# Kernel optimization log

Measured on AMD Instinct MI355X. Metric: run time of the kernel, lower is better.

The kernel has to match this reference:

```python
import jax, jax.numpy as jnp
import numpy as np
import math

H = 512       # hidden_dim
NL = 4        # num_layers
N2 = 32       # d_state // 2
B, L = 8, 4096
DT_MIN, DT_MAX = 1e-3, 1e-1
EPS = 1e-5


def _layer_norm(x, gamma, beta):
    mu = jnp.mean(x, axis=-1, keepdims=True)
    var = jnp.mean(jnp.square(x - mu), axis=-1, keepdims=True)
    return (x - mu) * jax.lax.rsqrt(var + EPS) * gamma + beta


def setup_inputs() -> dict:
    key = jax.random.key(0)
    ks = jax.random.split(key, 8)
    x = jax.random.normal(ks[0], (B, L, H), dtype=jnp.float32)
    # S4DKernel buffers / params, stacked over layers
    log_dt = jax.random.uniform(ks[1], (NL, H)) * (math.log(DT_MAX) - math.log(DT_MIN)) + math.log(DT_MIN)
    A_imag = jnp.broadcast_to(math.pi * jnp.arange(N2, dtype=jnp.float32), (NL, H, N2)).copy()
    log_A_real = jnp.full((NL, H, N2), math.log(0.5), dtype=jnp.float32)
    C = jax.random.normal(ks[2], (NL, H, N2, 2), dtype=jnp.float32)  # view_as_real of cfloat
    D = jax.random.normal(ks[3], (NL, H), dtype=jnp.float32)
    # 1x1 Conv1d h -> 2h (pointwise linear over channels)
    W = jax.random.normal(ks[4], (NL, 2 * H, H), dtype=jnp.float32) / math.sqrt(H)
    b = jax.random.normal(ks[5], (NL, 2 * H), dtype=jnp.float32) * 0.01
    gamma = jnp.ones((NL, H), dtype=jnp.float32)
    beta = jnp.zeros((NL, H), dtype=jnp.float32)
    return dict(x=x, log_dt=log_dt, A_imag=A_imag, log_A_real=log_A_real,
                C=C, D=D, W=W, b=b, gamma=gamma, beta=beta)


def reference(x, log_dt, A_imag, log_A_real, C, D, W, b, gamma, beta):
    Bsz, Lseq, h = x.shape
    t = jnp.arange(Lseq, dtype=jnp.float32)
    for i in range(NL):
        # --- S4D kernel generation ---
        dt = jnp.exp(log_dt[i])                                    # (h,)
        Cc = C[i, ..., 0] + 1j * C[i, ..., 1]                      # (h, n)
        A = -jnp.exp(log_A_real[i]) + 1j * A_imag[i]               # (h, n)
        dA = A * dt[:, None]                                       # (h, n)
        Cmod = Cc * (jnp.exp(dA) - 1.0) / A                        # (h, n)
        # Vandermonde: exp(dA * l), reduced over state dim
        K = 2.0 * jnp.einsum('hn,hnl->hl', Cmod,
                             jnp.exp(dA[:, :, None] * t)).real     # (h, L)
        # --- FFT long convolution ---
        u = jnp.transpose(x, (0, 2, 1))                            # (B, h, L)
        kf = jnp.fft.rfft(K, n=2 * Lseq)                           # (h, L+1)
        uf = jnp.fft.rfft(u, n=2 * Lseq)                           # (B, h, L+1)
        y = jnp.fft.irfft(uf * kf, n=2 * Lseq)[..., :Lseq]         # (B, h, L)
        y = y + u * D[i][:, None]
        y = jax.nn.gelu(y, approximate=False)                      # torch nn.GELU default (erf)
        # 1x1 conv h -> 2h then GLU over channel dim
        z = jnp.einsum('oh,bhl->bol', W[i], y) + b[i][None, :, None]
        a, g = jnp.split(z, 2, axis=1)
        y = a * jax.nn.sigmoid(g)                                  # (B, h, L)
        y = jnp.transpose(y, (0, 2, 1))                            # (B, L, h)
        x = _layer_norm(y + x, gamma[i], beta[i])
    return x
```

## Files before the change

kernel.cpp:

```cpp
#include <hip/hip_runtime.h>
#include <hip/hip_bf16.h>
#include <math.h>

#define H 512
#define NL 4
#define N2 32
#define Bsz 8
#define Lseq 4096
#define BT (Bsz*Lseq)
#define LC2 64
#define NCC (BT/LC2)
#define CPB (Lseq/LC2)

typedef __attribute__((ext_vector_type(8))) short short8;
typedef __attribute__((ext_vector_type(4))) float float4v;


__device__ __forceinline__ float bf2f(unsigned short u) {
    union { unsigned int i; float f; } x; x.i = ((unsigned int)u) << 16; return x.f;
}
__device__ __forceinline__ unsigned short f2bf(float f) {
    union { float f; unsigned int i; } x; x.f = f;
    unsigned int u = x.i + 0x7fff + ((x.i >> 16) & 1);
    return (unsigned short)(u >> 16);
}
__device__ __forceinline__ uint2 pack4bf(float a, float b, float c, float d) {
    uint2 r;
    r.x = (unsigned)f2bf(a) | ((unsigned)f2bf(b) << 16);
    r.y = (unsigned)f2bf(c) | ((unsigned)f2bf(d) << 16);
    return r;
}
__device__ __forceinline__ void async_copy16(const void* g, void* l) {
    __builtin_amdgcn_global_load_lds(
        (const __attribute__((address_space(1))) void*)g,
        (__attribute__((address_space(3))) void*)l, 16, 0, 0);
}

__global__ void wconv_kernel(const float* __restrict__ W, unsigned short* __restrict__ Wbf) {
    int tid = blockIdx.x * 256 + threadIdx.x;
    Wbf[tid] = f2bf(W[tid]);
}

__global__ void params_kernel(const float* __restrict__ log_dt, const float* __restrict__ A_imag,
                              const float* __restrict__ log_A_real, const float* __restrict__ Cin,
                              float* __restrict__ dA, float* __restrict__ Ct) {
    int tid = blockIdx.x * 256 + threadIdx.x;
    int h = tid % H;
    int n = (tid / H) % N2;
    int layer = tid / (H * N2);
    float dt = expf(log_dt[layer * H + h]);
    int pidx = (layer * H + h) * N2 + n;
    float Are = -expf(log_A_real[pidx]);
    float Aim = A_imag[pidx];
    float dre = Are * dt, dim = Aim * dt;
    float er = expf(dre);
    float lre = er * cosf(dim), lim = er * sinf(dim);
    float nre = lre - 1.0f, nim = lim;
    float inv = 1.0f / (Are * Are + Aim * Aim);
    float tre = (nre * Are + nim * Aim) * inv;
    float tim = (nim * Are - nre * Aim) * inv;
    float Ccre = Cin[pidx * 2], Ccim = Cin[pidx * 2 + 1];
    int oidx = ((layer * N2 + n) * 2) * H + h;
    dA[oidx] = dre;  dA[oidx + H] = dim;
    Ct[oidx] = 2.0f * (Ccre * tre - Ccim * tim);
    Ct[oidx + H] = 2.0f * (Ccre * tim + Ccim * tre);
}

__global__ void kergen_k_kernel(const float* __restrict__ dA, const float* __restrict__ Ct,
                                unsigned short* __restrict__ kmat) {
    int t = blockIdx.x * 256 + threadIdx.x;
    int d = t & 63;
    int h = (t >> 6) & (H - 1);
    int layer = t >> 15;
    float fd = (float)d;
    float sum = 0.f;
    for (int n = 0; n < N2; n++) {
        int base = ((layer * N2 + n) * 2) * H + h;
        float dre = dA[base], dim = dA[base + H];
        float Ctr = Ct[base], Cti = Ct[base + H];
        float e = expf(dre * fd);
        sum += Ctr * e * cosf(dim * fd) - Cti * e * sinf(dim * fd);
    }
    kmat[t] = f2bf(sum);
}

__global__ void kergenW_kernel(const float* __restrict__ dA, unsigned short* __restrict__ Wst, int layer) {
    int t = blockIdx.x * 256 + threadIdx.x;
    int j = t & 63;
    int r = (t >> 6) & 63;
    int h = t >> 12;
    int n = r >> 1;
    int base = ((layer * N2 + n) * 2) * H + h;
    float dre = dA[base], dim = dA[base + H];
    float p = (float)(63 - j);
    float e = expf(dre * p);
    Wst[t] = f2bf((r & 1) ? e * sinf(dim * p) : e * cosf(dim * p));
}

__global__ void kergenV_kernel(const float* __restrict__ dA, const float* __restrict__ Ct,
                               unsigned short* __restrict__ Vl, int layer) {
    int t = blockIdx.x * 256 + threadIdx.x;
    int c2 = t & 63;
    int l = (t >> 6) & 63;
    int h = t >> 12;
    int n = c2 >> 1;
    int base = ((layer * N2 + n) * 2) * H + h;
    float dre = dA[base], dim = dA[base + H];
    float Ctr = Ct[base], Cti = Ct[base + H];
    float q = (float)(l + 1);
    float e = expf(dre * q);
    float ar = e * cosf(dim * q), ai = e * sinf(dim * q);
    float vre = Ctr * ar - Cti * ai;
    float vim = Ctr * ai + Cti * ar;
    Vl[t] = f2bf((c2 & 1) ? -vim : vre);
}

__global__ __launch_bounds__(256) void t1_f32_kernel(const float* __restrict__ xi,
                                                     unsigned short* __restrict__ ut) {
    __shared__ float tile[64][68];
    int bx = blockIdx.x;
    int pt = bx & 511, ht = bx >> 9;
    int p0 = pt * 64, h0 = ht * 64;
    int t = threadIdx.x;
    int jr = t & 15, ib = t >> 4;
#pragma unroll
    for (int pass = 0; pass < 4; pass++) {
        int i = ib + pass * 16;
        float4 v = *(const float4*)(xi + (size_t)(p0 + i) * H + h0 + jr * 4);
        *(float4*)(&tile[i][jr * 4]) = v;
    }
    __syncthreads();
#pragma unroll
    for (int pass = 0; pass < 4; pass++) {
        int i2 = ib + pass * 16;
        int j2 = jr * 4;
        uint2 pk = pack4bf(tile[j2][i2], tile[j2 + 1][i2], tile[j2 + 2][i2], tile[j2 + 3][i2]);
        *(uint2*)(ut + (size_t)(h0 + i2) * BT + p0 + j2) = pk;
    }
}

__global__ __launch_bounds__(256) void states_kernel(const unsigned short* __restrict__ ut,
                                                     const unsigned short* __restrict__ Wst,
                                                     unsigned short* __restrict__ Sloc) {
    int h = blockIdx.x;
    int wave = threadIdx.x >> 6, lane = threadIdx.x & 63;
    int r16 = lane & 15, quad = lane >> 4;
    const unsigned short* uh = ut + (size_t)h * BT;
    const unsigned short* wh = Wst + (size_t)h * 64 * 64;
    unsigned short* sh = Sloc + (size_t)h * NCC * 64;
    for (int nt = 0; nt < 8; nt++) {
        int cc0 = wave * 128 + nt * 16;
        float4v acc[4] = {};
#pragma unroll
        for (int k0 = 0; k0 < 64; k0 += 32) {
            short8 bf = *reinterpret_cast<const short8*>(uh + (size_t)(cc0 + r16) * 64 + k0 + quad * 8);
#pragma unroll
            for (int mt = 0; mt < 4; mt++) {
                short8 af = *reinterpret_cast<const short8*>(wh + (mt * 16 + r16) * 64 + k0 + quad * 8);
                acc[mt] = __builtin_amdgcn_mfma_f32_16x16x32_bf16(af, bf, acc[mt], 0, 0, 0);
            }
        }
        int cc = cc0 + r16;
#pragma unroll
        for (int mt = 0; mt < 4; mt++) {
            uint2 pk = pack4bf(acc[mt][0], acc[mt][1], acc[mt][2], acc[mt][3]);
            *(uint2*)(sh + (size_t)cc * 64 + mt * 16 + quad * 4) = pk;
        }
    }
}

__global__ void combine_kernel(unsigned short* __restrict__ Sloc, const float* __restrict__ dA, int layer) {
    int t = blockIdx.x * 256 + threadIdx.x;
    int n = t & 31;
    int b = (t >> 5) & 7;
    int h = t >> 8;
    int base = ((layer * N2 + n) * 2) * H + h;
    float dre = dA[base], dim = dA[base + H];
    float e = expf(dre * 64.f);
    float Lr = e * cosf(dim * 64.f), Li = e * sinf(dim * 64.f);
    unsigned int* p = (unsigned int*)Sloc + ((size_t)h * NCC + b * CPB) * 32 + n;
    float sr = 0.f, si = 0.f;
    for (int c = 0; c < CPB; c++) {
        unsigned int v = p[(size_t)c * 32];
        float pr = bf2f(v & 0xffff), pi = bf2f(v >> 16);
        p[(size_t)c * 32] = (unsigned)f2bf(sr) | ((unsigned)f2bf(si) << 16);
        float nr = fmaf(Lr, sr, fmaf(-Li, si, pr));
        float ni = fmaf(Lr, si, fmaf(Li, sr, pi));
        sr = nr; si = ni;
    }
}

__global__ __launch_bounds__(256) void conv_kernel(const unsigned short* __restrict__ ut,
                                                   const unsigned short* __restrict__ kmat,
                                                   const unsigned short* __restrict__ Vl,
                                                   const unsigned short* __restrict__ Sent,
                                                   const float* __restrict__ Dp,
                                                   unsigned short* __restrict__ yt, int layer) {
    __shared__ unsigned short T[64][72];
    int h = blockIdx.x, half = blockIdx.y;
    int t = threadIdx.x;
    const unsigned short* km = kmat + ((size_t)layer * H + h) * 64;
    {
        int l = t >> 2, j0 = (t & 3) * 16;
#pragma unroll
        for (int g = 0; g < 2; g++) {
            short8 v;
#pragma unroll
            for (int e = 0; e < 8; e++) {
                int j = j0 + g * 8 + e;
                v[e] = (j <= l) ? (short)km[l - j] : (short)0;
            }
            *reinterpret_cast<short8*>(&T[l][j0 + g * 8]) = v;
        }
    }
    __syncthreads();
    int wave = t >> 6, lane = t & 63;
    int r16 = lane & 15, quad = lane >> 4;
    const unsigned short* uh = ut + (size_t)h * BT;
    const unsigned short* vh = Vl + (size_t)h * 64 * 64;
    const unsigned short* eh = Sent + (size_t)h * NCC * 64;
    unsigned short* yh = yt + (size_t)h * BT;
    float Dh = Dp[layer * H + h];
    for (int nt = 0; nt < 4; nt++) {
        int cc0 = half * 256 + wave * 64 + nt * 16;
        float4v acc[4] = {};
#pragma unroll
        for (int k0 = 0; k0 < 64; k0 += 32) {
            short8 bf = *reinterpret_cast<const short8*>(uh + (size_t)(cc0 + r16) * 64 + k0 + quad * 8);
#pragma unroll
            for (int mt = 0; mt < 4; mt++) {
                short8 af = *reinterpret_cast<const short8*>(&T[mt * 16 + r16][k0 + quad * 8]);
                acc[mt] = __builtin_amdgcn_mfma_f32_16x16x32_bf16(af, bf, acc[mt], 0, 0, 0);
            }
        }
#pragma unroll
        for (int k0 = 0; k0 < 64; k0 += 32) {
            short8 bf = *reinterpret_cast<const short8*>(eh + (size_t)(cc0 + r16) * 64 + k0 + quad * 8);
#pragma unroll
            for (int mt = 0; mt < 4; mt++) {
                short8 af = *reinterpret_cast<const short8*>(vh + (mt * 16 + r16) * 64 + k0 + quad * 8);
                acc[mt] = __builtin_amdgcn_mfma_f32_16x16x32_bf16(af, bf, acc[mt], 0, 0, 0);
            }
        }
        int cc = cc0 + r16;
#pragma unroll
        for (int mt = 0; mt < 4; mt++) {
            size_t p = (size_t)cc * 64 + mt * 16 + quad * 4;
            ushort4 uu = *(const ushort4*)(uh + p);
            float o[4];
#pragma unroll
            for (int r = 0; r < 4; r++) {
                float y = acc[mt][r] + Dh * bf2f(((const unsigned short*)&uu)[r]);
                o[r] = 0.5f * y * (1.0f + erff(y * 0.70710678118654752f));
            }
            *(uint2*)(yh + p) = pack4bf(o[0], o[1], o[2], o[3]);
        }
    }
}

__global__ __launch_bounds__(256) void transpose2_kernel(const unsigned short* __restrict__ yt,
                                                         unsigned short* __restrict__ yb) {
    __shared__ unsigned short tile[64][72];
    int bx = blockIdx.x;
    int pt = bx & 511, ht = bx >> 9;
    int p0 = pt * 64, h0 = ht * 64;
    int t = threadIdx.x;
    int jr = t & 7, ib = t >> 3;
#pragma unroll
    for (int pass = 0; pass < 2; pass++) {
        int i = ib + pass * 32;
        short8 v = *reinterpret_cast<const short8*>(yt + (size_t)(h0 + i) * BT + p0 + jr * 8);
        *reinterpret_cast<short8*>(&tile[i][jr * 8]) = v;
    }
    __syncthreads();
    int pp = t >> 2, hg = t & 3;
    short8 o0, o1;
#pragma unroll
    for (int r = 0; r < 8; r++) o0[r] = (short)tile[hg * 16 + r][pp];
#pragma unroll
    for (int r = 0; r < 8; r++) o1[r] = (short)tile[hg * 16 + 8 + r][pp];
    unsigned short* dst = yb + (size_t)(p0 + pp) * H + h0 + hg * 16;
    *reinterpret_cast<short8*>(dst) = o0;
    *reinterpret_cast<short8*>(dst + 8) = o1;
}

__global__ __launch_bounds__(256) void gemm_glu_kernel(const unsigned short* __restrict__ ybf,
                                                       const unsigned short* __restrict__ Wbf,
                                                       const float* __restrict__ bias,
                                                       unsigned short* __restrict__ yo, int layer) {
    __shared__ unsigned short As[3][128 * 32];
    __shared__ unsigned short Bs[3][128 * 32];
    int tid = threadIdx.x;
    int wave = tid >> 6, lane = tid & 63;
    int wr = wave >> 1, wc = wave & 1;
    int r16 = lane & 15, quad = lane >> 4;
    int m0 = blockIdx.x * 128;
    int o0 = blockIdx.y * 64;
    const unsigned short* Wl = Wbf + (size_t)layer * 2 * H * H;

    int srow = lane >> 2;
    int scol = ((lane & 3) ^ ((srow >> 1) & 3)) * 8;
    const unsigned short* aS0 = ybf + ((size_t)(m0 + wave * 16 + srow)) * H + scol;
    const unsigned short* aS1 = aS0 + (size_t)64 * H;
    const unsigned short* bSA = Wl + ((size_t)(o0 + wave * 16 + srow)) * H + scol;
    const unsigned short* bSG = bSA + (size_t)512 * H;
    const int aoff0 = (wave * 16) * 32;
    const int aoff1 = (64 + wave * 16) * 32;

    int rcol = (quad ^ ((r16 >> 1) & 3)) * 8;

    float4v acc_a[4][2] = {}, acc_g[4][2] = {};

    async_copy16(aS0,      &As[0][aoff0]);
    async_copy16(aS1,      &As[0][aoff1]);
    async_copy16(bSA,      &Bs[0][aoff0]);
    async_copy16(bSG,      &Bs[0][aoff1]);
    async_copy16(aS0 + 32, &As[1][aoff0]);
    async_copy16(aS1 + 32, &As[1][aoff1]);
    async_copy16(bSA + 32, &Bs[1][aoff0]);
    async_copy16(bSG + 32, &Bs[1][aoff1]);
    asm volatile("s_waitcnt vmcnt(4)" ::: "memory");
    __builtin_amdgcn_s_barrier();

#pragma unroll
    for (int ks = 0; ks < 16; ++ks) {
        const int b = ks % 3;
        if (ks < 14) {
            const int nb = (ks + 2) % 3;
            const int kn = (ks + 2) * 32;
            async_copy16(aS0 + kn, &As[nb][aoff0]);
            async_copy16(aS1 + kn, &As[nb][aoff1]);
            async_copy16(bSA + kn, &Bs[nb][aoff0]);
            async_copy16(bSG + kn, &Bs[nb][aoff1]);
        }

        short8 af[4], ba[2], bg[2];
#pragma unroll
        for (int mi = 0; mi < 4; mi++)
            af[mi] = *reinterpret_cast<const short8*>(&As[b][(wr * 64 + mi * 16 + r16) * 32 + rcol]);
#pragma unroll
        for (int ni = 0; ni < 2; ni++) {
            ba[ni] = *reinterpret_cast<const short8*>(&Bs[b][(wc * 32 + ni * 16 + r16) * 32 + rcol]);
            bg[ni] = *reinterpret_cast<const short8*>(&Bs[b][(64 + wc * 32 + ni * 16 + r16) * 32 + rcol]);
        }
#pragma unroll
        for (int mi = 0; mi < 4; mi++)
#pragma unroll
            for (int ni = 0; ni < 2; ni++) {
                acc_a[mi][ni] = __builtin_amdgcn_mfma_f32_16x16x32_bf16(af[mi], ba[ni], acc_a[mi][ni], 0, 0, 0);
                acc_g[mi][ni] = __builtin_amdgcn_mfma_f32_16x16x32_bf16(af[mi], bg[ni], acc_g[mi][ni], 0, 0, 0);
            }

        if (ks < 14) {
            asm volatile("s_waitcnt vmcnt(4) lgkmcnt(0)" ::: "memory");
            __builtin_amdgcn_s_barrier();
        } else if (ks == 14) {
            asm volatile("s_waitcnt vmcnt(0) lgkmcnt(0)" ::: "memory");
            __builtin_amdgcn_s_barrier();
        }
    }

    const float* bl = bias + layer * 2 * H;
#pragma unroll
    for (int ni = 0; ni < 2; ni++) {
        int o = o0 + wc * 32 + ni * 16 + r16;
        float ba_ = bl[o], bg_ = bl[H + o];
#pragma unroll
        for (int mi = 0; mi < 4; mi++)
#pragma unroll
            for (int r = 0; r < 4; r++) {
                int l = m0 + wr * 64 + mi * 16 + quad * 4 + r;
                float av = acc_a[mi][ni][r] + ba_;
                float gv = acc_g[mi][ni][r] + bg_;
                yo[(size_t)l * H + o] = f2bf(av * (1.0f / (1.0f + expf(-gv))));
            }
    }
}

__global__ __launch_bounds__(256) void ln_t_kernel(const unsigned short* __restrict__ yo,
                                                   const float* __restrict__ xf,
                                                   const unsigned short* __restrict__ xb,
                                                   const float* __restrict__ gamma,
                                                   const float* __restrict__ beta,
                                                   unsigned short* __restrict__ xR,
                                                   unsigned short* __restrict__ ut,
                                                   int in_f32, int layer) {
    __shared__ unsigned short tl[64][520];
    int t = threadIdx.x;
    int p0 = blockIdx.x * 64;
    int lane8 = t & 7;
    int rowb = t >> 3;
    const float* gl = gamma + layer * H;
    const float* bl = beta + layer * H;
#pragma unroll
    for (int rr = 0; rr < 2; rr++) {
        int row = rowb + rr * 32;
        size_t gbase = (size_t)(p0 + row) * H;
        float v[64];
        float s = 0.f, s2 = 0.f;
#pragma unroll
        for (int cc = 0; cc < 8; cc++) {
            int h0 = (lane8 + cc * 8) * 8;
            short8 yv = *reinterpret_cast<const short8*>(yo + gbase + h0);
            if (in_f32) {
                float4 x0 = *(const float4*)(xf + gbase + h0);
                float4 x1 = *(const float4*)(xf + gbase + h0 + 4);
                v[cc * 8 + 0] = bf2f((unsigned short)yv[0]) + x0.x;
                v[cc * 8 + 1] = bf2f((unsigned short)yv[1]) + x0.y;
                v[cc * 8 + 2] = bf2f((unsigned short)yv[2]) + x0.z;
                v[cc * 8 + 3] = bf2f((unsigned short)yv[3]) + x0.w;
                v[cc * 8 + 4] = bf2f((unsigned short)yv[4]) + x1.x;
                v[cc * 8 + 5] = bf2f((unsigned short)yv[5]) + x1.y;
                v[cc * 8 + 6] = bf2f((unsigned short)yv[6]) + x1.z;
                v[cc * 8 + 7] = bf2f((unsigned short)yv[7]) + x1.w;
            } else {
                short8 xv = *reinterpret_cast<const short8*>(xb + gbase + h0);
#pragma unroll
                for (int i = 0; i < 8; i++)
                    v[cc * 8 + i] = bf2f((unsigned short)yv[i]) + bf2f((unsigned short)xv[i]);
            }
#pragma unroll
            for (int i = 0; i < 8; i++) { s += v[cc * 8 + i]; s2 = fmaf(v[cc * 8 + i], v[cc * 8 + i], s2); }
        }
        s += __shfl_xor(s, 1);  s2 += __shfl_xor(s2, 1);
        s += __shfl_xor(s, 2);  s2 += __shfl_xor(s2, 2);
        s += __shfl_xor(s, 4);  s2 += __shfl_xor(s2, 4);
        float mu = s * (1.0f / H);
        float var = s2 * (1.0f / H) - mu * mu;
        float inv = rsqrtf(var + 1e-5f);
#pragma unroll
        for (int cc = 0; cc < 8; cc++) {
            int h0 = (lane8 + cc * 8) * 8;
            float4 g0 = *(const float4*)(gl + h0);
            float4 g1 = *(const float4*)(gl + h0 + 4);
            float4 b0 = *(const float4*)(bl + h0);
            float4 b1 = *(const float4*)(bl + h0 + 4);
            short8 pk;
            pk[0] = (short)f2bf((v[cc * 8 + 0] - mu) * inv * g0.x + b0.x);
            pk[1] = (short)f2bf((v[cc * 8 + 1] - mu) * inv * g0.y + b0.y);
            pk[2] = (short)f2bf((v[cc * 8 + 2] - mu) * inv * g0.z + b0.z);
            pk[3] = (short)f2bf((v[cc * 8 + 3] - mu) * inv * g0.w + b0.w);
            pk[4] = (short)f2bf((v[cc * 8 + 4] - mu) * inv * g1.x + b1.x);
            pk[5] = (short)f2bf((v[cc * 8 + 5] - mu) * inv * g1.y + b1.y);
            pk[6] = (short)f2bf((v[cc * 8 + 6] - mu) * inv * g1.z + b1.z);
            pk[7] = (short)f2bf((v[cc * 8 + 7] - mu) * inv * g1.w + b1.w);
            *reinterpret_cast<short8*>(xR + gbase + h0) = pk;
            *reinterpret_cast<short8*>(&tl[row][h0]) = pk;
        }
    }
    __syncthreads();
#pragma unroll
    for (int hh = 0; hh < 2; hh++) {
        int h = t + hh * 256;
        unsigned short* dst = ut + (size_t)h * BT + p0;
#pragma unroll
        for (int pc = 0; pc < 8; pc++) {
            short8 o;
#pragma unroll
            for (int e = 0; e < 8; e++) o[e] = (short)tl[pc * 8 + e][h];
            *reinterpret_cast<short8*>(dst + pc * 8) = o;
        }
    }
}

__global__ __launch_bounds__(256) void ln_kernel(const unsigned short* __restrict__ yo,
                                                 const float* __restrict__ xf,
                                                 const unsigned short* __restrict__ xb,
                                                 const float* __restrict__ gamma, const float* __restrict__ beta,
                                                 float* __restrict__ of, unsigned short* __restrict__ ob,
                                                 int in_f32, int out_f32, int layer) {
    int wave = threadIdx.x >> 6, lane = threadIdx.x & 63;
    size_t row = (size_t)blockIdx.x * 4 + wave;
    const unsigned short* yp = yo + row * H + lane * 8;
    short8 yv = *reinterpret_cast<const short8*>(yp);
    float v[8];
    if (in_f32) {
        const float* xp = xf + row * H + lane * 8;
        float4 x0 = *(const float4*)(xp);
        float4 x1 = *(const float4*)(xp + 4);
        v[0] = bf2f((unsigned short)yv[0]) + x0.x; v[1] = bf2f((unsigned short)yv[1]) + x0.y;
        v[2] = bf2f((unsigned short)yv[2]) + x0.z; v[3] = bf2f((unsigned short)yv[3]) + x0.w;
        v[4] = bf2f((unsigned short)yv[4]) + x1.x; v[5] = bf2f((unsigned short)yv[5]) + x1.y;
        v[6] = bf2f((unsigned short)yv[6]) + x1.z; v[7] = bf2f((unsigned short)yv[7]) + x1.w;
    } else {
        const unsigned short* xp = xb + row * H + lane * 8;
        short8 xv = *reinterpret_cast<const short8*>(xp);
#pragma unroll
        for (int i = 0; i < 8; i++)
            v[i] = bf2f((unsigned short)yv[i]) + bf2f((unsigned short)xv[i]);
    }
    float s = 0.f, s2 = 0.f;
#pragma unroll
    for (int i = 0; i < 8; i++) { s += v[i]; s2 = fmaf(v[i], v[i], s2); }
#pragma unroll
    for (int off = 32; off; off >>= 1) {
        s += __shfl_xor(s, off);
        s2 += __shfl_xor(s2, off);
    }
    float mu = s * (1.0f / H);
    float var = s2 * (1.0f / H) - mu * mu;
    float inv = rsqrtf(var + 1e-5f);
    const float* gl = gamma + layer * H + lane * 8;
    const float* bl = beta + layer * H + lane * 8;
    float o[8];
#pragma unroll
    for (int i = 0; i < 8; i++)
        o[i] = (v[i] - mu) * inv * gl[i] + bl[i];
    if (out_f32) {
        float* op = of + row * H + lane * 8;
        *(float4*)(op) = make_float4(o[0], o[1], o[2], o[3]);
        *(float4*)(op + 4) = make_float4(o[4], o[5], o[6], o[7]);
    } else {
        unsigned short* op = ob + row * H + lane * 8;
        uint2 p0 = pack4bf(o[0], o[1], o[2], o[3]);
        uint2 p1 = pack4bf(o[4], o[5], o[6], o[7]);
        *(uint2*)(op) = p0;
        *(uint2*)(op + 4) = p1;
    }
}

extern "C" void kernel_launch(void* const* d_in, const int* in_sizes, int n_in,
                              void* d_out, int out_size, void* d_ws, size_t ws_size,
                              hipStream_t stream) {
    const float* x          = (const float*)d_in[0];
    const float* log_dt     = (const float*)d_in[1];
    const float* A_imag     = (const float*)d_in[2];
    const float* log_A_real = (const float*)d_in[3];
    const float* C          = (const float*)d_in[4];
    const float* D          = (const float*)d_in[5];
    const float* W          = (const float*)d_in[6];
    const float* bias       = (const float*)d_in[7];
    const float* gamma      = (const float*)d_in[8];
    const float* beta       = (const float*)d_in[9];

    char* ws = (char*)d_ws;
    unsigned short* xR   = (unsigned short*)(ws + 0);
    unsigned short* Sloc = (unsigned short*)(ws + 67108864);
    unsigned short* u_t  = (unsigned short*)(ws + 100663296);
    unsigned short* ybf  = (unsigned short*)(ws + 100663296);
    unsigned short* y_t  = (unsigned short*)(ws + 134217728);
    unsigned short* yo   = (unsigned short*)(ws + 134217728);
    unsigned short* Wbf  = (unsigned short*)(ws + 167772160);
    unsigned short* WV   = (unsigned short*)(ws + 171966464);
    unsigned short* kmat = (unsigned short*)(ws + 176160768);
    float*          dA   = (float*)(ws + 176422912);
    float*          Ct   = (float*)(ws + 176947200);
    float* xout_final    = (float*)d_out;

    wconv_kernel<<<NL * 2 * H * H / 256, 256, 0, stream>>>(W, Wbf);
    params_kernel<<<NL * N2 * H / 256, 256, 0, stream>>>(log_dt, A_imag, log_A_real, C, dA, Ct);
    kergen_k_kernel<<<NL * H * 64 / 256, 256, 0, stream>>>(dA, Ct, kmat);

    for (int layer = 0; layer < NL; ++layer) {
        if (layer == 0)
            t1_f32_kernel<<<4096, 256, 0, stream>>>(x, u_t);
        kergenW_kernel<<<H * 64 * 64 / 256, 256, 0, stream>>>(dA, WV, layer);
        states_kernel<<<H, 256, 0, stream>>>(u_t, WV, Sloc);
        combine_kernel<<<H * Bsz * N2 / 256, 256, 0, stream>>>(Sloc, dA, layer);
        kergenV_kernel<<<H * 64 * 64 / 256, 256, 0, stream>>>(dA, Ct, WV, layer);
        conv_kernel<<<dim3(H, 2), 256, 0, stream>>>(u_t, kmat, WV, Sloc, D, y_t, layer);
        transpose2_kernel<<<4096, 256, 0, stream>>>(y_t, ybf);
        gemm_glu_kernel<<<dim3(BT / 128, H / 64), 256, 0, stream>>>(ybf, Wbf, bias, yo, layer);
        if (layer < NL - 1) {
            ln_t_kernel<<<BT / 64, 256, 0, stream>>>(yo, x, xR, gamma, beta,
                                                     xR, u_t, (layer == 0) ? 1 : 0, layer);
        } else {
            ln_kernel<<<BT / 4, 256, 0, stream>>>(yo, x, xR, gamma, beta,
                                                  xout_final, xR, 0, 1, layer);
        }
    }
}
```

Baseline: 854.3 us.

## Fuse chunk-state, scan combine and convolution into one per-(channel,batch) SSM kernel

Replaces the separate states, combine and conv kernels with a single ssm_kernel launched per channel and batch. Chunk-local states are computed with MFMA into shared memory, one wave runs the serial complex scan across the 64 chunks (real/imag pairs split over lanes and exchanged with shuffles), and the result feeds the intra/inter-chunk MFMA convolution directly. This removes the global Sloc round trips and two launches. In exchange, the scan runs serially on a single wave while the other waves wait at a barrier, and W and V now need separate buffers.

Result: no change. 841.3 us (-1.5%).

```diff
diff --git a/kernel.cpp b/kernel.cpp
--- a/kernel.cpp
+++ b/kernel.cpp
@@ -139,65 +139,17 @@
     }
 }
 
-__global__ __launch_bounds__(256) void states_kernel(const unsigned short* __restrict__ ut,
-                                                     const unsigned short* __restrict__ Wst,
-                                                     unsigned short* __restrict__ Sloc) {
-    int h = blockIdx.x;
-    int wave = threadIdx.x >> 6, lane = threadIdx.x & 63;
-    int r16 = lane & 15, quad = lane >> 4;
-    const unsigned short* uh = ut + (size_t)h * BT;
-    const unsigned short* wh = Wst + (size_t)h * 64 * 64;
-    unsigned short* sh = Sloc + (size_t)h * NCC * 64;
-    for (int nt = 0; nt < 8; nt++) {
-        int cc0 = wave * 128 + nt * 16;
-        float4v acc[4] = {};
-#pragma unroll
-        for (int k0 = 0; k0 < 64; k0 += 32) {
-            short8 bf = *reinterpret_cast<const short8*>(uh + (size_t)(cc0 + r16) * 64 + k0 + quad * 8);
-#pragma unroll
-            for (int mt = 0; mt < 4; mt++) {
-                short8 af = *reinterpret_cast<const short8*>(wh + (mt * 16 + r16) * 64 + k0 + quad * 8);
-                acc[mt] = __builtin_amdgcn_mfma_f32_16x16x32_bf16(af, bf, acc[mt], 0, 0, 0);
-            }
-        }
-        int cc = cc0 + r16;
-#pragma unroll
-        for (int mt = 0; mt < 4; mt++) {
-            uint2 pk = pack4bf(acc[mt][0], acc[mt][1], acc[mt][2], acc[mt][3]);
-            *(uint2*)(sh + (size_t)cc * 64 + mt * 16 + quad * 4) = pk;
-        }
-    }
-}
-
-__global__ void combine_kernel(unsigned short* __restrict__ Sloc, const float* __restrict__ dA, int layer) {
-    int t = blockIdx.x * 256 + threadIdx.x;
-    int n = t & 31;
-    int b = (t >> 5) & 7;
-    int h = t >> 8;
-    int base = ((layer * N2 + n) * 2) * H + h;
-    float dre = dA[base], dim = dA[base + H];
-    float e = expf(dre * 64.f);
-    float Lr = e * cosf(dim * 64.f), Li = e * sinf(dim * 64.f);
-    unsigned int* p = (unsigned int*)Sloc + ((size_t)h * NCC + b * CPB) * 32 + n;
-    float sr = 0.f, si = 0.f;
-    for (int c = 0; c < CPB; c++) {
-        unsigned int v = p[(size_t)c * 32];
-        float pr = bf2f(v & 0xffff), pi = bf2f(v >> 16);
-        p[(size_t)c * 32] = (unsigned)f2bf(sr) | ((unsigned)f2bf(si) << 16);
-        float nr = fmaf(Lr, sr, fmaf(-Li, si, pr));
-        float ni = fmaf(Lr, si, fmaf(Li, sr, pi));
-        sr = nr; si = ni;
-    }
-}
-
-__global__ __launch_bounds__(256) void conv_kernel(const unsigned short* __restrict__ ut,
-                                                   const unsigned short* __restrict__ kmat,
-                                                   const unsigned short* __restrict__ Vl,
-                                                   const unsigned short* __restrict__ Sent,
-                                                   const float* __restrict__ Dp,
-                                                   unsigned short* __restrict__ yt, int layer) {
+__global__ __launch_bounds__(256) void ssm_kernel(const unsigned short* __restrict__ ut,
+                                                  const unsigned short* __restrict__ kmat,
+                                                  const unsigned short* __restrict__ Wst,
+                                                  const unsigned short* __restrict__ Vl,
+                                                  const float* __restrict__ dA,
+                                                  const float* __restrict__ Dp,
+                                                  unsigned short* __restrict__ yt, int layer) {
     __shared__ unsigned short T[64][72];
-    int h = blockIdx.x, half = blockIdx.y;
+    __shared__ unsigned short Sl[64][72];
+    __shared__ unsigned short El[64][72];
+    int h = blockIdx.x, b = blockIdx.y;
     int t = threadIdx.x;
     const unsigned short* km = kmat + ((size_t)layer * H + h) * 64;
     {
@@ -213,16 +165,53 @@
             *reinterpret_cast<short8*>(&T[l][j0 + g * 8]) = v;
         }
     }
-    __syncthreads();
     int wave = t >> 6, lane = t & 63;
     int r16 = lane & 15, quad = lane >> 4;
-    const unsigned short* uh = ut + (size_t)h * BT;
+    const unsigned short* uh = ut + (size_t)h * BT + (size_t)b * Lseq;
+    const unsigned short* wh = Wst + (size_t)h * 64 * 64;
     const unsigned short* vh = Vl + (size_t)h * 64 * 64;
-    const unsigned short* eh = Sent + (size_t)h * NCC * 64;
-    unsigned short* yh = yt + (size_t)h * BT;
-    float Dh = Dp[layer * H + h];
-    for (int nt = 0; nt < 4; nt++) {
-        int cc0 = half * 256 + wave * 64 + nt * 16;
+
+    {
+        int cc0 = wave * 16;
+        float4v acc[4] = {};
+#pragma unroll
+        for (int k0 = 0; k0 < 64; k0 += 32) {
+            short8 bf = *reinterpret_cast<const short8*>(uh + (size_t)(cc0 + r16) * 64 + k0 + quad * 8);
+#pragma unroll
+            for (int mt = 0; mt < 4; mt++) {
+                short8 af = *reinterpret_cast<const short8*>(wh + (mt * 16 + r16) * 64 + k0 + quad * 8);
+                acc[mt] = __builtin_amdgcn_mfma_f32_16x16x32_bf16(af, bf, acc[mt], 0, 0, 0);
+            }
+        }
+        int cc = cc0 + r16;
+#pragma unroll
+        for (int mt = 0; mt < 4; mt++) {
+            uint2 pk = pack4bf(acc[mt][0], acc[mt][1], acc[mt][2], acc[mt][3]);
+            *(uint2*)(&Sl[cc][mt * 16 + quad * 4]) = pk;
+        }
+    }
+    __syncthreads();
+
+    if (wave == 0) {
+        int r = lane;
+        int n = r >> 1;
+        int base = ((layer * N2 + n) * 2) * H + h;
+        float dre = dA[base], dim = dA[base + H];
+        float e = expf(dre * 64.f);
+        float Lr = e * cosf(dim * 64.f), Li = e * sinf(dim * 64.f);
+        float Ls = (r & 1) ? Li : -Li;
+        float s = 0.f;
+        for (int c = 0; c < 64; c++) {
+            El[c][r] = f2bf(s);
+            float p = bf2f(Sl[c][r]);
+            float sp = __shfl_xor(s, 1);
+            s = fmaf(Lr, s, fmaf(Ls, sp, p));
+        }
+    }
+    __syncthreads();
+
+    {
+        int cc0 = wave * 16;
         float4v acc[4] = {};
 #pragma unroll
         for (int k0 = 0; k0 < 64; k0 += 32) {
@@ -235,14 +224,16 @@
         }
 #pragma unroll
         for (int k0 = 0; k0 < 64; k0 += 32) {
-            short8 bf = *reinterpret_cast<const short8*>(eh + (size_t)(cc0 + r16) * 64 + k0 + quad * 8);
+            short8 bf = *reinterpret_cast<const short8*>(&El[cc0 + r16][k0 + quad * 8]);
 #pragma unroll
             for (int mt = 0; mt < 4; mt++) {
                 short8 af = *reinterpret_cast<const short8*>(vh + (mt * 16 + r16) * 64 + k0 + quad * 8);
                 acc[mt] = __builtin_amdgcn_mfma_f32_16x16x32_bf16(af, bf, acc[mt], 0, 0, 0);
             }
         }
+        float Dh = Dp[layer * H + h];
         int cc = cc0 + r16;
+        unsigned short* yh = yt + (size_t)h * BT + (size_t)b * Lseq;
 #pragma unroll
         for (int mt = 0; mt < 4; mt++) {
             size_t p = (size_t)cc * 64 + mt * 16 + quad * 4;
@@ -535,13 +526,13 @@
 
     char* ws = (char*)d_ws;
     unsigned short* xR   = (unsigned short*)(ws + 0);
-    unsigned short* Sloc = (unsigned short*)(ws + 67108864);
+    unsigned short* Vbuf = (unsigned short*)(ws + 67108864);
     unsigned short* u_t  = (unsigned short*)(ws + 100663296);
     unsigned short* ybf  = (unsigned short*)(ws + 100663296);
     unsigned short* y_t  = (unsigned short*)(ws + 134217728);
     unsigned short* yo   = (unsigned short*)(ws + 134217728);
     unsigned short* Wbf  = (unsigned short*)(ws + 167772160);
-    unsigned short* WV   = (unsigned short*)(ws + 171966464);
+    unsigned short* Wstb = (unsigned short*)(ws + 171966464);
     unsigned short* kmat = (unsigned short*)(ws + 176160768);
     float*          dA   = (float*)(ws + 176422912);
     float*          Ct   = (float*)(ws + 176947200);
@@ -554,11 +545,9 @@
     for (int layer = 0; layer < NL; ++layer) {
         if (layer == 0)
             t1_f32_kernel<<<4096, 256, 0, stream>>>(x, u_t);
-        kergenW_kernel<<<H * 64 * 64 / 256, 256, 0, stream>>>(dA, WV, layer);
-        states_kernel<<<H, 256, 0, stream>>>(u_t, WV, Sloc);
-        combine_kernel<<<H * Bsz * N2 / 256, 256, 0, stream>>>(Sloc, dA, layer);
-        kergenV_kernel<<<H * 64 * 64 / 256, 256, 0, stream>>>(dA, Ct, WV, layer);
-        conv_kernel<<<dim3(H, 2), 256, 0, stream>>>(u_t, kmat, WV, Sloc, D, y_t, layer);
+        kergenW_kernel<<<H * 64 * 64 / 256, 256, 0, stream>>>(dA, Wstb, layer);
+        kergenV_kernel<<<H * 64 * 64 / 256, 256, 0, stream>>>(dA, Ct, Vbuf, layer);
+        ssm_kernel<<<dim3(H, Bsz), 256, 0, stream>>>(u_t, kmat, Wstb, Vbuf, dA, D, y_t, layer);
         transpose2_kernel<<<4096, 256, 0, stream>>>(y_t, ybf);
         gemm_glu_kernel<<<dim3(BT / 128, H / 64), 256, 0, stream>>>(ybf, Wbf, bias, yo, layer);
         if (layer < NL - 1) {
```
